# Kernel tuning notes

Hardware: AMD Instinct MI355X
Metric: run time of the kernel (lower is better)

Reference implementation:

```python
import jax, jax.numpy as jnp
import numpy as np

H, KVH, D, R = 32, 8, 128, 32
MASK_OUT = 0.5
NEG = -1e9  # stand-in for finfo.min to avoid -inf accumulation; preserves ordering/softmax
ROPE_THETA = 10000.0


def _rope_tables(S, D):
    inv = 1.0 / (ROPE_THETA ** (np.arange(0, D, 2, dtype=np.float32) / D))
    t = np.arange(S, dtype=np.float32)
    freqs = np.outer(t, inv)
    emb = np.concatenate([freqs, freqs], axis=-1)  # [S, D]
    return jnp.asarray(np.cos(emb)), jnp.asarray(np.sin(emb))


def _apply_rope(x, cos, sin):
    # x: [B,H,S,D]; cos/sin: [S,D]
    x1, x2 = jnp.split(x, 2, axis=-1)
    rot = jnp.concatenate([-x2, x1], axis=-1)
    return x * cos[None, None] + rot * sin[None, None]


def setup_inputs() -> dict:
    B, S, E = 1, 1024, 4096
    key = jax.random.key(0)
    ks = jax.random.split(key, 9)
    n = lambda k, shp, sc=0.02: jax.random.normal(k, shp, jnp.float32) * sc
    return {
        'hidden_states': n(ks[0], (B, S, E), 1.0),
        'wq': n(ks[1], (E, H * D)),
        'wk': n(ks[2], (E, KVH * D)),
        'wv': n(ks[3], (E, KVH * D)),
        'wo': n(ks[4], (H * D, E)),
        'mixq': n(ks[5], (E, R)),
        'mixk': n(ks[6], (E, R)),
        'q_pos': n(ks[7], (S, H, R, D)),
        'k_pos': n(ks[8], (S, H, R, D)),
    }


def reference(hidden_states, wq, wk, wv, wo, mixq, mixk, q_pos, k_pos):
    B, S, E = hidden_states.shape
    rep = H // KVH
    # QKV projections -> [B, heads, S, D]
    q = (hidden_states @ wq).reshape(B, S, H, D).transpose(0, 2, 1, 3)
    k = (hidden_states @ wk).reshape(B, S, KVH, D).transpose(0, 2, 1, 3)
    v = (hidden_states @ wv).reshape(B, S, KVH, D).transpose(0, 2, 1, 3)
    k = jnp.repeat(k, rep, axis=1)  # repeat_kv (GQA expand) -> [B,H,S,D]
    v = jnp.repeat(v, rep, axis=1)

    cos, sin = _rope_tables(S, D)
    qr = _apply_rope(q, cos, sin)
    kr = _apply_rope(k, cos, sin)
    scale = 1.0 / jnp.sqrt(jnp.float32(D))
    true_score = jnp.einsum('bhqd,bhkd->bhqk', qr, kr) * scale  # [B,H,S,S]

    # low-rank position-dependent draft score
    lrq = hidden_states @ mixq  # [B,S,R]
    lrk = hidden_states @ mixk
    pq = jnp.einsum('bmr,mhrd->bhmd', lrq, q_pos)  # [B,H,S,D]
    pk = jnp.einsum('bnr,nhrd->bhnd', lrk, k_pos)
    draft_score = jnp.einsum('bhqd,bhkd->bhqk', pq, pk)  # [B,H,S,S]

    causal = jnp.where(jnp.tril(jnp.ones((S, S), dtype=bool)), 0.0, NEG).astype(jnp.float32)[None, None]
    draft_score = draft_score + causal  # prefill: add causal mask to draft score

    num_remain = S - int(S * MASK_OUT)
    _, draft_idx = jax.lax.top_k(draft_score, num_remain)  # [B,H,S,K]

    # scatter 0 at kept kv positions, NEG elsewhere
    bi = jnp.arange(B)[:, None, None, None]
    hi = jnp.arange(H)[None, :, None, None]
    qi = jnp.arange(S)[None, None, :, None]
    topk_mask = jnp.full((B, H, S, S), NEG, jnp.float32).at[bi, hi, qi, draft_idx].set(0.0)

    probs = jax.nn.softmax(true_score + causal + topk_mask, axis=-1)
    out = jnp.einsum('bhqk,bhkd->bqhd', probs, v).reshape(B, S, H * D)
    return out @ wo
```

## Files before the change

### kernel.cpp

```cpp
#include <hip/hip_runtime.h>
#include <hip/hip_bf16.h>
#include <math.h>


typedef unsigned short u16;
typedef unsigned long long u64;
using bf16x8 = __attribute__((ext_vector_type(8))) short;
using f32x4  = __attribute__((ext_vector_type(4))) float;

#define NEGBIG -1e30f
#define QSCALE 0.08838834764831845f

__device__ __forceinline__ unsigned int fkey(float f) {
    unsigned int u = __float_as_uint(f);
    return (u & 0x80000000u) ? ~u : (u | 0x80000000u);
}

__device__ __forceinline__ u16 f2b(float f) {
    union { float f; unsigned u; } x; x.f = f;
    unsigned r = x.u + 0x7fffu + ((x.u >> 16) & 1u);
    return (u16)(r >> 16);
}

__device__ __forceinline__ void gl_lds16(const u16* g, u16* l) {
    __builtin_amdgcn_global_load_lds(
        (__attribute__((address_space(1))) void*)(g),
        (__attribute__((address_space(3))) void*)(l), 16, 0, 0);
}

__device__ __forceinline__ void rope_table_calc(int row, int i,
    float* __restrict__ cosb, float* __restrict__ sinb)
{
    double inv = pow(10000.0, -((double)(2 * i)) / 128.0);
    double ang = (double)row * inv;
    cosb[row * 64 + i] = (float)cos(ang);
    sinb[row * 64 + i] = (float)sin(ang);
}

__global__ __launch_bounds__(256) void init_kernel(
    const float* __restrict__ hs, u16* __restrict__ hs_bf,
    float* __restrict__ cosb, float* __restrict__ sinb)
{
    int bx = blockIdx.x, t = threadIdx.x;
    if (bx < 4096) {
        int i = bx * 256 + t;
        float4 v = ((const float4*)hs)[i];
        u16 o[4] = {f2b(v.x), f2b(v.y), f2b(v.z), f2b(v.w)};
        ((uint2*)hs_bf)[i] = *(const uint2*)o;
    } else {
        rope_table_calc((bx - 4096) * 4 + (t >> 6), t & 63, cosb, sinb);
    }
}

__device__ __forceinline__ void transpose_tile(
    const float* __restrict__ in, u16* __restrict__ out, int Kdim, int N,
    int bx, int by)
{
    __shared__ u16 tile[64][66];
    int n0 = bx * 64, k0 = by * 64;
    int t = threadIdx.x;
#pragma unroll
    for (int u = 0; u < 16; ++u) {
        int e = u * 256 + t; int r = e >> 6, c = e & 63;
        tile[r][c] = f2b(in[(size_t)(k0 + r) * N + n0 + c]);
    }
    __syncthreads();
#pragma unroll
    for (int u = 0; u < 16; ++u) {
        int e = u * 256 + t; int r = e >> 6, c = e & 63;
        out[(size_t)(n0 + r) * Kdim + k0 + c] = tile[c][r];
    }
}

__global__ __launch_bounds__(256) void transpose_bf16_kernel(
    const float* __restrict__ in, u16* __restrict__ out, int Kdim, int N)
{
    transpose_tile(in, out, Kdim, N, blockIdx.x, blockIdx.y);
}

__global__ __launch_bounds__(256) void transpose_qkvw_kernel(
    const float* __restrict__ wq, const float* __restrict__ wk, const float* __restrict__ wv,
    u16* __restrict__ wqT, u16* __restrict__ wkT, u16* __restrict__ wvT)
{
    int bx = blockIdx.x;
    const float* in; u16* outp; int N;
    if (bx < 64)      { in = wq; outp = wqT; N = 4096; }
    else if (bx < 80) { in = wk; outp = wkT; N = 1024; bx -= 64; }
    else              { in = wv; outp = wvT; N = 1024; bx -= 80; }
    transpose_tile(in, outp, 4096, N, bx, blockIdx.y);
}

__global__ __launch_bounds__(256) void init_fused_kernel(
    const float* __restrict__ hs, u16* __restrict__ hs_bf,
    float* __restrict__ cosb, float* __restrict__ sinb,
    const float* __restrict__ mixq, const float* __restrict__ mixk,
    float* __restrict__ lrq, float* __restrict__ lrk,
    const float* __restrict__ wq, const float* __restrict__ wk, const float* __restrict__ wv,
    u16* __restrict__ wqT, u16* __restrict__ wkT, u16* __restrict__ wvT)
{
    __shared__ float row[4096];
    __shared__ float part[2][32][4];
    int bx = blockIdx.x, t = threadIdx.x;
    if (bx < 4096) {
        int i = bx * 256 + t;
        float4 v = ((const float4*)hs)[i];
        u16 o[4] = {f2b(v.x), f2b(v.y), f2b(v.z), f2b(v.w)};
        ((uint2*)hs_bf)[i] = *(const uint2*)o;
    } else if (bx < 4352) {
        rope_table_calc((bx - 4096) * 4 + (t >> 6), t & 63, cosb, sinb);
    } else if (bx < 5376) {
        int m = bx - 4352;
#pragma unroll
        for (int u = 0; u < 4; ++u)
            ((float4*)row)[t + u * 256] = ((const float4*)(hs + (size_t)m * 4096))[t + u * 256];
        __syncthreads();
        int r = t & 31, which = (t >> 5) & 1, quarter = t >> 6;
        const float* mix = which ? mixk : mixq;
        float acc = 0.f;
        int kbase = quarter * 1024;
#pragma unroll 8
        for (int kk = 0; kk < 1024; ++kk)
            acc = fmaf(row[kbase + kk], mix[(size_t)(kbase + kk) * 32 + r], acc);
        part[which][r][quarter] = acc;
        __syncthreads();
        if (t < 64) {
            int r2 = t & 31, w2 = t >> 5;
            float s = part[w2][r2][0] + part[w2][r2][1] + part[w2][r2][2] + part[w2][r2][3];
            (w2 ? lrk : lrq)[(size_t)m * 32 + r2] = s;
        }
    } else {
        int idx = bx - 5376;
        int bxT = idx % 96, byT = idx / 96;
        const float* in; u16* outp; int N;
        if (bxT < 64)      { in = wq; outp = wqT; N = 4096; }
        else if (bxT < 80) { in = wk; outp = wkT; N = 1024; bxT -= 64; }
        else               { in = wv; outp = wvT; N = 1024; bxT -= 80; }
        transpose_tile(in, outp, 4096, N, bxT, byT);
    }
}

__global__ __launch_bounds__(128) void rope_pack2_kernel(
    const float* __restrict__ qb, const float* __restrict__ kb,
    const float* __restrict__ cosb, const float* __restrict__ sinb,
    u16* __restrict__ qr, u16* __restrict__ kr)
{
    int s = blockIdx.x, h = blockIdx.y, d = threadIdx.x;
    const float* src; u16* dst; int W; float scale;
    if (h < 32) { src = qb; dst = qr; W = 4096; scale = QSCALE; }
    else        { h -= 32; src = kb; dst = kr; W = 1024; scale = 1.0f; }
    float x  = src[(size_t)s * W + h * 128 + d];
    float x2 = src[(size_t)s * W + h * 128 + (d ^ 64)];
    float cs = cosb[s * 64 + (d & 63)];
    float sn = sinb[s * 64 + (d & 63)];
    float rot = (d < 64) ? -x2 : x2;
    dst[((size_t)h * 1024 + s) * 128 + d] = f2b((x * cs + rot * sn) * scale);
}

__global__ __launch_bounds__(256) void reduce_rope_v_kernel(
    const float* __restrict__ C0, const float* __restrict__ C1,
    const float* __restrict__ cosb, const float* __restrict__ sinb,
    u16* __restrict__ qr, u16* __restrict__ kr, u16* __restrict__ vT)
{
    __shared__ u16 tile[64][66];
    int bx = blockIdx.x, t = threadIdx.x;
    if (bx < 20480) {
        int sp = bx & 511, h40 = bx >> 9;
        int s = sp * 2 + (t >> 7), d = t & 127;
        int col; u16* dst; float scale;
        if (h40 < 32) { col = h40 * 128 + d; dst = qr + ((size_t)h40 * 1024 + s) * 128 + d; scale = QSCALE; }
        else { col = 4096 + (h40 - 32) * 128 + d; dst = kr + ((size_t)(h40 - 32) * 1024 + s) * 128 + d; scale = 1.0f; }
        int colp = col ^ 64;
        float x  = C0[(size_t)s * 6144 + col]  + C1[(size_t)s * 6144 + col];
        float x2 = C0[(size_t)s * 6144 + colp] + C1[(size_t)s * 6144 + colp];
        float cs = cosb[s * 64 + (d & 63)];
        float sn = sinb[s * 64 + (d & 63)];
        float rot = (d < 64) ? -x2 : x2;
        *dst = f2b((x * cs + rot * sn) * scale);
    } else {
        int idx = bx - 20480;
        int bxT = idx & 15, byT = idx >> 4;
        int n0 = bxT * 64, k0 = byT * 64;
#pragma unroll
        for (int u = 0; u < 16; ++u) {
            int e = u * 256 + t; int r = e >> 6, c = e & 63;
            size_t off = (size_t)(k0 + r) * 6144 + 5120 + n0 + c;
            tile[r][c] = f2b(C0[off] + C1[off]);
        }
        __syncthreads();
#pragma unroll
        for (int u = 0; u < 16; ++u) {
            int e = u * 256 + t; int r = e >> 6, c = e & 63;
            vT[(size_t)(n0 + r) * 1024 + k0 + c] = tile[c][r];
        }
    }
}

__global__ __launch_bounds__(256) void reduce_out_kernel(
    const float* __restrict__ D0, const float* __restrict__ D1, float* __restrict__ out)
{
    int i = blockIdx.x * 256 + threadIdx.x;
    float4 a = ((const float4*)D0)[i];
    float4 b = ((const float4*)D1)[i];
    ((float4*)out)[i] = make_float4(a.x + b.x, a.y + b.y, a.z + b.z, a.w + b.w);
}

__device__ __forceinline__ void gemm_bf16_panel(
    const u16* __restrict__ Ap,
    const u16* __restrict__ Bp,
    float* __restrict__ Cp,
    int Kdim, int kbase, int klen, int Cst)
{
    __shared__ u16 As[128 * 32];
    __shared__ u16 Bs[128 * 32];
    const int t = threadIdx.x;
    const int wave = t >> 6, lane = t & 63;
    const int wr = wave >> 1, wc = wave & 1;
    const int fr = lane & 15, fq = lane >> 4;

    f32x4 acc[4][4];
#pragma unroll
    for (int m = 0; m < 4; ++m)
#pragma unroll
        for (int n = 0; n < 4; ++n) acc[m][n] = 0.f;

    const int srow = 32 * wave + (lane >> 2);
    const int skc = (lane & 3) * 8;
    const u16* aS = Ap + (size_t)srow * Kdim + kbase + skc;
    const u16* bS = Bp + (size_t)srow * Kdim + kbase + skc;
    u16* aD0 = As + 1024 * wave;  u16* aD1 = aD0 + 512;
    u16* bD0 = Bs + 1024 * wave;  u16* bD1 = bD0 + 512;

    const int aoff = (wr * 64 + fr) * 32 + fq * 8;
    const int boff = (wc * 64 + fr) * 32 + fq * 8;

    for (int k0 = 0; k0 < klen; k0 += 32) {
        __syncthreads();
        gl_lds16(aS + k0, aD0);
        gl_lds16(aS + (size_t)16 * Kdim + k0, aD1);
        gl_lds16(bS + k0, bD0);
        gl_lds16(bS + (size_t)16 * Kdim + k0, bD1);
        __syncthreads();

        bf16x8 af[4], bfr[4];
#pragma unroll
        for (int m = 0; m < 4; ++m) af[m] = *(const bf16x8*)(As + aoff + m * 512);
#pragma unroll
        for (int n = 0; n < 4; ++n) bfr[n] = *(const bf16x8*)(Bs + boff + n * 512);
#pragma unroll
        for (int m = 0; m < 4; ++m)
#pragma unroll
            for (int n = 0; n < 4; ++n)
                acc[m][n] = __builtin_amdgcn_mfma_f32_16x16x32_bf16(af[m], bfr[n], acc[m][n], 0, 0, 0);
    }

    float* Cb = Cp + (size_t)(wr * 64 + fq * 4) * Cst + wc * 64 + fr;
#pragma unroll
    for (int m = 0; m < 4; ++m)
#pragma unroll
        for (int j = 0; j < 4; ++j)
#pragma unroll
            for (int n = 0; n < 4; ++n)
                Cb[(size_t)(m * 16 + j) * Cst + n * 16] = acc[m][n][j];
}

__global__ __launch_bounds__(256) void gemm_qkv_bf16_kernel(
    const u16* __restrict__ hs_bf, const u16* __restrict__ wqT,
    const u16* __restrict__ wkT, const u16* __restrict__ wvT,
    float* __restrict__ q, float* __restrict__ k, float* __restrict__ v)
{
    int bn = blockIdx.x, bm = blockIdx.y;
    const u16* Bsel; float* Csel; int Ncols;
    if (bn < 32)      { Bsel = wqT; Csel = q; Ncols = 4096; }
    else if (bn < 40) { Bsel = wkT; Csel = k; Ncols = 1024; bn -= 32; }
    else              { Bsel = wvT; Csel = v; Ncols = 1024; bn -= 40; }
    gemm_bf16_panel(hs_bf + (size_t)bm * 128 * 4096, Bsel + (size_t)bn * 128 * 4096,
                    Csel + (size_t)bm * 128 * Ncols + bn * 128, 4096, 0, 4096, Ncols);
}

__global__ __launch_bounds__(256) void gemm_wo_bf16_kernel(
    const u16* __restrict__ attn_bf, const u16* __restrict__ woT, float* __restrict__ out)
{
    int bn = blockIdx.x, bm = blockIdx.y;
    gemm_bf16_panel(attn_bf + (size_t)bm * 128 * 4096, woT + (size_t)bn * 128 * 4096,
                    out + (size_t)bm * 128 * 4096 + bn * 128, 4096, 0, 4096, 4096);
}

__global__ __launch_bounds__(256) void gemm_qkv_sk_kernel(
    const u16* __restrict__ hs_bf, const u16* __restrict__ wqT,
    const u16* __restrict__ wkT, const u16* __restrict__ wvT,
    float* __restrict__ C0, float* __restrict__ C1)
{
    int bn = blockIdx.x, bm = blockIdx.y, g = blockIdx.z;
    const u16* Bsel; int bnrow;
    if (bn < 32)      { Bsel = wqT; bnrow = bn; }
    else if (bn < 40) { Bsel = wkT; bnrow = bn - 32; }
    else              { Bsel = wvT; bnrow = bn - 40; }
    float* C = g ? C1 : C0;
    gemm_bf16_panel(hs_bf + (size_t)bm * 128 * 4096, Bsel + (size_t)bnrow * 128 * 4096,
                    C + (size_t)bm * 128 * 6144 + bn * 128, 4096, g * 2048, 2048, 6144);
}

__global__ __launch_bounds__(256) void gemm_wo_sk_kernel(
    const u16* __restrict__ attn_bf, const u16* __restrict__ woT,
    float* __restrict__ D0, float* __restrict__ D1)
{
    int bn = blockIdx.x, bm = blockIdx.y, g = blockIdx.z;
    float* C = g ? D1 : D0;
    gemm_bf16_panel(attn_bf + (size_t)bm * 128 * 4096, woT + (size_t)bn * 128 * 4096,
                    C + (size_t)bm * 128 * 4096 + bn * 128, 4096, g * 2048, 2048, 4096);
}

__global__ __launch_bounds__(256) void lr_kernel(
    const float* __restrict__ hs, const float* __restrict__ mixq, const float* __restrict__ mixk,
    float* __restrict__ lrq, float* __restrict__ lrk)
{
    __shared__ float row[4096];
    __shared__ float part[2][32][4];
    int m = blockIdx.x, t = threadIdx.x;
#pragma unroll
    for (int u = 0; u < 4; ++u)
        ((float4*)row)[t + u * 256] = ((const float4*)(hs + (size_t)m * 4096))[t + u * 256];
    __syncthreads();
    int r = t & 31, which = (t >> 5) & 1, quarter = t >> 6;
    const float* mix = which ? mixk : mixq;
    float acc = 0.f;
    int kbase = quarter * 1024;
#pragma unroll 8
    for (int kk = 0; kk < 1024; ++kk)
        acc = fmaf(row[kbase + kk], mix[(size_t)(kbase + kk) * 32 + r], acc);
    part[which][r][quarter] = acc;
    __syncthreads();
    if (t < 64) {
        int r2 = t & 31, w2 = t >> 5;
        float s = part[w2][r2][0] + part[w2][r2][1] + part[w2][r2][2] + part[w2][r2][3];
        (w2 ? lrk : lrq)[(size_t)m * 32 + r2] = s;
    }
}

__global__ __launch_bounds__(128) void ppos2_kernel(
    const float* __restrict__ lrq, const float* __restrict__ lrk,
    const float* __restrict__ qpos, const float* __restrict__ kpos,
    float* __restrict__ pq, float* __restrict__ pk)
{
    int h = blockIdx.x, by = blockIdx.y, d = threadIdx.x;
    const float* lr; const float* pos; float* outp; int m;
    if (by < 512) { m = 512 + by; lr = lrq; pos = qpos; outp = pq; }
    else          { m = by - 512; lr = lrk; pos = kpos; outp = pk; }
    __shared__ float lrs[32];
    if (d < 32) lrs[d] = lr[(size_t)m * 32 + d];
    __syncthreads();
    const float* base = pos + ((size_t)(m * 32 + h) * 32) * 128 + d;
    float acc = 0.f;
#pragma unroll
    for (int r = 0; r < 32; ++r)
        acc = fmaf(lrs[r], base[(size_t)r * 128], acc);
    outp[((size_t)h * 1024 + m) * 128 + d] = acc;
}

__global__ __launch_bounds__(256) void draft_gemm_kernel(
    const float* __restrict__ pq, const float* __restrict__ pk,
    float* __restrict__ scores, int h0)
{
    int idx = blockIdx.x;
    int bm, bc;
    if (idx < 10)      { bm = 4; bc = idx; }
    else if (idx < 22) { bm = 5; bc = idx - 10; }
    else if (idx < 36) { bm = 6; bc = idx - 22; }
    else               { bm = 7; bc = idx - 36; }
    int hh = blockIdx.y;

    const float* A  = pq + ((size_t)(h0 + hh) * 1024 + bm * 128) * 128;
    const float* BT = pk + ((size_t)(h0 + hh) * 1024 + bc * 64) * 128;
    float* C = scores + ((size_t)hh * 512 + (bm - 4) * 128) * 1024 + bc * 64;

    __shared__ float As[8][128];
    __shared__ float Bs[8][64];
    const int t = threadIdx.x;
    const int tx = t & 15, ty = (t >> 4) & 15;

    float acc[8][4];
#pragma unroll
    for (int u = 0; u < 8; ++u)
#pragma unroll
        for (int w = 0; w < 4; ++w) acc[u][w] = 0.f;

    const int ai = t >> 1, ah = (t & 1) * 4;
    const int bi = t >> 2, bh = (t & 3) * 2;
    const float* Ap = A + (size_t)ai * 128 + ah;
    const float* Bp = BT + (size_t)bi * 128 + bh;

    for (int k0 = 0; k0 < 128; k0 += 8) {
        float4 av = *(const float4*)(Ap + k0);
        float2 bv = *(const float2*)(Bp + k0);
        __syncthreads();
        As[ah + 0][ai] = av.x; As[ah + 1][ai] = av.y;
        As[ah + 2][ai] = av.z; As[ah + 3][ai] = av.w;
        Bs[bh][bi] = bv.x; Bs[bh + 1][bi] = bv.y;
        __syncthreads();
#pragma unroll
        for (int kk = 0; kk < 8; ++kk) {
            float4 a0 = *(const float4*)(&As[kk][ty * 4]);
            float4 a1 = *(const float4*)(&As[kk][64 + ty * 4]);
            float4 b0 = *(const float4*)(&Bs[kk][tx * 4]);
            float aa[8] = {a0.x, a0.y, a0.z, a0.w, a1.x, a1.y, a1.z, a1.w};
#pragma unroll
            for (int u = 0; u < 8; ++u) {
                acc[u][0] = fmaf(aa[u], b0.x, acc[u][0]);
                acc[u][1] = fmaf(aa[u], b0.y, acc[u][1]);
                acc[u][2] = fmaf(aa[u], b0.z, acc[u][2]);
                acc[u][3] = fmaf(aa[u], b0.w, acc[u][3]);
            }
        }
    }
#pragma unroll
    for (int u = 0; u < 8; ++u) {
        int row = (u < 4) ? (ty * 4 + u) : (64 + ty * 4 + (u - 4));
        *(float4*)(C + (size_t)row * 1024 + tx * 4)
            = make_float4(acc[u][0], acc[u][1], acc[u][2], acc[u][3]);
    }
}

__global__ __launch_bounds__(256) void topk_select_kernel(
    const float* __restrict__ scores, int h0,
    unsigned long long* __restrict__ mask)
{
    int qt = blockIdx.x, hh = blockIdx.y;
    int h = h0 + hh;
    int t = threadIdx.x;
    const int i = t >> 4, jj = t & 15;
    const int lrow = qt * 16 + i;
    const int qrow = 512 + lrow;

    const float* src = scores + ((size_t)hh * 512 + lrow) * 1024;

    unsigned int vals[64];
#pragma unroll
    for (int g = 0; g < 16; ++g) {
        float4 v = *(const float4*)(src + g * 64 + jj * 4);
        int col = g * 64 + jj * 4;
        vals[g * 4 + 0] = fkey((col + 0) <= qrow ? v.x : NEGBIG);
        vals[g * 4 + 1] = fkey((col + 1) <= qrow ? v.y : NEGBIG);
        vals[g * 4 + 2] = fkey((col + 2) <= qrow ? v.z : NEGBIG);
        vals[g * 4 + 3] = fkey((col + 3) <= qrow ? v.w : NEGBIG);
    }

    unsigned int p = 0u;
    int kth = 512;
    for (int b = 31; b >= 0; --b) {
        unsigned int bit = 1u << b;
        unsigned int himask = (b == 31) ? 0u : (0xFFFFFFFFu << (b + 1));
        int cnt = 0;
#pragma unroll
        for (int n = 0; n < 64; ++n)
            cnt += (int)((((vals[n] ^ p) & himask) == 0u) && ((vals[n] & bit) != 0u));
        cnt += __shfl_xor(cnt, 1);
        cnt += __shfl_xor(cnt, 2);
        cnt += __shfl_xor(cnt, 4);
        cnt += __shfl_xor(cnt, 8);
        if (cnt >= kth) p |= bit; else kth -= cnt;
    }

    unsigned long long wpart[16];
#pragma unroll
    for (int w = 0; w < 16; ++w) wpart[w] = 0ull;
#pragma unroll
    for (int g = 0; g < 16; ++g)
#pragma unroll
        for (int e = 0; e < 4; ++e)
            wpart[g] |= ((unsigned long long)(vals[g * 4 + e] >= p)) << (4 * jj + e);
#pragma unroll
    for (int s = 1; s < 16; s <<= 1) {
#pragma unroll
        for (int w = 0; w < 16; ++w)
            wpart[w] |= __shfl_xor(wpart[w], s);
    }
    mask[((size_t)h * 1024 + qrow) * 16 + jj] = wpart[jj];
}

#define ATTN_KP 136
#define ATTN_VP 72

__global__ __launch_bounds__(256) void attn_mfma_kernel(
    const u16* __restrict__ qr, const u16* __restrict__ kr,
    const u16* __restrict__ vT,
    const unsigned long long* __restrict__ mask,
    u16* __restrict__ attn)
{
    int bx = blockIdx.x;
    int qt = (bx & 1) ? (bx >> 1) : (15 - (bx >> 1));
    int h = blockIdx.y;
    int kvh = h >> 2;
    int q0 = qt * 64;
    int t = threadIdx.x;
    int wave = t >> 6, lane = t & 63;
    int fr = lane & 15, fq = lane >> 4;
    int qrow = q0 + wave * 16 + fr;

    __shared__ u16 Ks[64 * ATTN_KP];
    __shared__ u16 Vs[128 * ATTN_VP];

    bf16x8 qf[4];
    const u16* qbase = qr + ((size_t)h * 1024 + qrow) * 128 + fq * 8;
#pragma unroll
    for (int kc = 0; kc < 4; ++kc)
        qf[kc] = *(const bf16x8*)(qbase + kc * 32);

    float m_run = -3.0e38f, l_run = 0.f;
    f32x4 accO[8];
#pragma unroll
    for (int m2 = 0; m2 < 8; ++m2) accO[m2] = 0.f;

    const unsigned long long* mrow = mask + ((size_t)h * 1024 + qrow) * 16;
    const bool use_mask = (qrow >= 512);
    const u16* kgh = kr + (size_t)kvh * 1024 * 128;
    const u16* vgh = vT + (size_t)kvh * 128 * 1024;

    int ntiles = qt + 1;
    for (int c = 0; c < ntiles; ++c) {
        int kv0 = c * 64;
        __syncthreads();
#pragma unroll
        for (int u = 0; u < 4; ++u) {
            int e = t + u * 256;
            int row = e >> 4, bc2 = (e & 15) * 8;
            uint4 d4 = *(const uint4*)(kgh + ((size_t)(kv0 + row)) * 128 + bc2);
            *(uint4*)(&Ks[row * ATTN_KP + bc2]) = d4;
        }
#pragma unroll
        for (int u = 0; u < 4; ++u) {
            int e = t + u * 256;
            int row = e >> 3, bc2 = (e & 7) * 8;
            uint4 d4 = *(const uint4*)(vgh + (size_t)row * 1024 + kv0 + bc2);
            *(uint4*)(&Vs[row * ATTN_VP + bc2]) = d4;
        }
        __syncthreads();

        f32x4 accS[4];
        accS[0] = 0.f; accS[1] = 0.f; accS[2] = 0.f; accS[3] = 0.f;
#pragma unroll
        for (int t2 = 0; t2 < 4; ++t2)
#pragma unroll
            for (int kc = 0; kc < 4; ++kc) {
                bf16x8 kf = *(const bf16x8*)(&Ks[(t2 * 16 + fr) * ATTN_KP + kc * 32 + fq * 8]);
                accS[t2] = __builtin_amdgcn_mfma_f32_16x16x32_bf16(kf, qf[kc], accS[t2], 0, 0, 0);
            }

        unsigned long long mw = use_mask ? mrow[c] : ~0ull;
        float p[4][4];
        float tmax = -3.0e38f;
#pragma unroll
        for (int t2 = 0; t2 < 4; ++t2)
#pragma unroll
            for (int j = 0; j < 4; ++j) {
                int kvi = (t2 << 4) + (fq << 2) + j;
                bool ok = ((mw >> kvi) & 1ull) && (kv0 + kvi <= qrow);
                float s = ok ? accS[t2][j] : -3.0e38f;
                p[t2][j] = s;
                tmax = fmaxf(tmax, s);
            }
// ... 5 lines not shown
#pragma unroll
        for (int t2 = 0; t2 < 4; ++t2)
#pragma unroll
            for (int j = 0; j < 4; ++j) {
                float e = (p[t2][j] > -1.0e38f) ? __expf(p[t2][j] - m_new) : 0.f;
                p[t2][j] = e;
                psum += e;
            }
        psum += __shfl_xor(psum, 16);
        psum += __shfl_xor(psum, 32);
        l_run = l_run * sf + psum;
        m_run = m_new;

#pragma unroll
        for (int m2 = 0; m2 < 8; ++m2) accO[m2] *= sf;

        union { uint4 u; bf16x8 b; } pc[2];
        int srcA = fr + ((fq & 1) << 5);
        int srcB = srcA + 16;
        bool hi = (fq & 2) != 0;
#pragma unroll
        for (int half = 0; half < 2; ++half) {
            unsigned W0, W1, W2, W3;
            asm("v_cvt_pk_bf16_f32 %0, %1, %2" : "=v"(W0) : "v"(p[2 * half][0]),     "v"(p[2 * half][1]));
            asm("v_cvt_pk_bf16_f32 %0, %1, %2" : "=v"(W1) : "v"(p[2 * half][2]),     "v"(p[2 * half][3]));
            asm("v_cvt_pk_bf16_f32 %0, %1, %2" : "=v"(W2) : "v"(p[2 * half + 1][0]), "v"(p[2 * half + 1][1]));
            asm("v_cvt_pk_bf16_f32 %0, %1, %2" : "=v"(W3) : "v"(p[2 * half + 1][2]), "v"(p[2 * half + 1][3]));
            unsigned a0 = __shfl(W0, srcA), a1 = __shfl(W1, srcA);
            unsigned a2 = __shfl(W2, srcA), a3 = __shfl(W3, srcA);
            unsigned b0 = __shfl(W0, srcB), b1 = __shfl(W1, srcB);
            unsigned b2 = __shfl(W2, srcB), b3 = __shfl(W3, srcB);
            pc[half].u.x = hi ? a2 : a0;
            pc[half].u.y = hi ? a3 : a1;
            pc[half].u.z = hi ? b2 : b0;
            pc[half].u.w = hi ? b3 : b1;
        }

#pragma unroll
        for (int m2 = 0; m2 < 8; ++m2) {
            bf16x8 vf0 = *(const bf16x8*)(&Vs[(m2 * 16 + fr) * ATTN_VP + fq * 8]);
            accO[m2] = __builtin_amdgcn_mfma_f32_16x16x32_bf16(vf0, pc[0].b, accO[m2], 0, 0, 0);
            bf16x8 vf1 = *(const bf16x8*)(&Vs[(m2 * 16 + fr) * ATTN_VP + 32 + fq * 8]);
            accO[m2] = __builtin_amdgcn_mfma_f32_16x16x32_bf16(vf1, pc[1].b, accO[m2], 0, 0, 0);
        }
    }

    float il = 1.0f / l_run;
    u16* obase = attn + (size_t)qrow * 4096 + h * 128 + fq * 4;
#pragma unroll
    for (int m2 = 0; m2 < 8; ++m2) {
        uint2 st;
        st.x = (unsigned)f2b(accO[m2][0] * il) | ((unsigned)f2b(accO[m2][1] * il) << 16);
        st.y = (unsigned)f2b(accO[m2][2] * il) | ((unsigned)f2b(accO[m2][3] * il) << 16);
        *(uint2*)(obase + m2 * 16) = st;
    }
}

extern "C" void kernel_launch(void* const* d_in, const int* in_sizes, int n_in,
                              void* d_out, int out_size, void* d_ws, size_t ws_size,
                              hipStream_t stream)
{
    (void)in_sizes; (void)n_in; (void)out_size;
    const float* hs   = (const float*)d_in[0];
    const float* wq   = (const float*)d_in[1];
    const float* wk   = (const float*)d_in[2];
    const float* wv   = (const float*)d_in[3];
    const float* wo   = (const float*)d_in[4];
    const float* mixq = (const float*)d_in[5];
    const float* mixk = (const float*)d_in[6];
    const float* qpos = (const float*)d_in[7];
    const float* kpos = (const float*)d_in[8];
    float* out = (float*)d_out;
    char* B = (char*)d_ws;
    const size_t MB = 1ull << 20;

    if (ws_size >= 123 * MB) {
        u16* hs_bf = (u16*)(B);
        u16* wkT   = (u16*)(B + 8 * MB);
        u16* wvT   = (u16*)(B + 16 * MB);
        u16* wqT   = (u16*)(B + 24 * MB);
        u16* qr    = (u16*)(B + 24 * MB);
        u16* kr    = (u16*)(B + 32 * MB);
        u16* vT    = (u16*)(B + 34 * MB);
        u16* woT   = (u16*)(B + 24 * MB);
        float* C0  = (float*)(B + 56 * MB);
        float* C1  = (float*)(B + 80 * MB);
        float* pq  = (float*)(B + 56 * MB);
        float* pk  = (float*)(B + 72 * MB);
        float* scores = (float*)(B + 88 * MB);
        float* D0  = (float*)(B + 56 * MB);
        float* D1  = (float*)(B + 72 * MB);
        u64* mask  = (u64*)(B + 120 * MB);
        float* lrq = (float*)(B + 122 * MB);
        float* lrk = lrq + 32768;
        float* cosb = lrk + 32768;
        float* sinb = cosb + 65536;
        u16* attn_bf = hs_bf;

        hipLaunchKernelGGL(init_fused_kernel, dim3(11520), dim3(256), 0, stream,
                           hs, hs_bf, cosb, sinb, mixq, mixk, lrq, lrk,
                           wq, wk, wv, wqT, wkT, wvT);
        hipLaunchKernelGGL(gemm_qkv_sk_kernel, dim3(48, 8, 2), dim3(256), 0, stream,
                           hs_bf, wqT, wkT, wvT, C0, C1);
        hipLaunchKernelGGL(reduce_rope_v_kernel, dim3(20736), dim3(256), 0, stream,
                           C0, C1, cosb, sinb, qr, kr, vT);
        hipLaunchKernelGGL(ppos2_kernel, dim3(32, 1536), dim3(128), 0, stream,
                           lrq, lrk, qpos, kpos, pq, pk);
        for (int h0 = 0; h0 < 32; h0 += 16) {
            hipLaunchKernelGGL(draft_gemm_kernel, dim3(52, 16), dim3(256), 0, stream,
                               pq, pk, scores, h0);
            hipLaunchKernelGGL(topk_select_kernel, dim3(32, 16), dim3(256), 0, stream,
                               scores, h0, mask);
        }
        hipLaunchKernelGGL(attn_mfma_kernel, dim3(16, 32), dim3(256), 0, stream,
                           qr, kr, vT, mask, attn_bf);
        hipLaunchKernelGGL(transpose_bf16_kernel, dim3(64, 64), dim3(256), 0, stream,
                           wo, woT, 4096, 4096);
        hipLaunchKernelGGL(gemm_wo_sk_kernel, dim3(32, 8, 2), dim3(256), 0, stream,
                           attn_bf, woT, D0, D1);
        hipLaunchKernelGGL(reduce_out_kernel, dim3(4096), dim3(256), 0, stream,
                           D0, D1, out);
    } else {
        float* ws   = (float*)d_ws;
        float* qb   = ws;
        float* kb   = qb + 4194304;
        float* vb   = kb + 1048576;
        float* pq   = vb + 1048576;
        float* pk   = pq + 4194304;
        float* lrq  = pk + 4194304;
        float* lrk  = lrq + 32768;
        float* cosb = lrk + 32768;
        float* sinb = cosb + 65536;
        u64* mask = (u64*)(sinb + 65536);
        u16* hs_bf = (u16*)(ws + 14876672 + 1048576);
        u16* wkT   = hs_bf + 4194304;
        u16* wvT   = wkT + 4194304;
        u16* wqT   = (u16*)pq;
        u16* woT   = (u16*)pq;
        u16* qr_bf = (u16*)pq;
        u16* kr_bf = (u16*)pk;
        u16* vT_bf = (u16*)(pk + 1048576);
        u16* attn_bf = hs_bf;
        float* scores = (float*)hs_bf;

        hipLaunchKernelGGL(init_kernel, dim3(4352), dim3(256), 0, stream, hs, hs_bf, cosb, sinb);
        hipLaunchKernelGGL(transpose_qkvw_kernel, dim3(96, 64), dim3(256), 0, stream,
                           wq, wk, wv, wqT, wkT, wvT);
        hipLaunchKernelGGL(gemm_qkv_bf16_kernel, dim3(48, 8), dim3(256), 0, stream,
                           hs_bf, wqT, wkT, wvT, qb, kb, vb);
        hipLaunchKernelGGL(lr_kernel, dim3(1024), dim3(256), 0, stream, hs, mixq, mixk, lrq, lrk);
        hipLaunchKernelGGL(ppos2_kernel, dim3(32, 1536), dim3(128), 0, stream,
                           lrq, lrk, qpos, kpos, pq, pk);
        for (int h0 = 0; h0 < 32; h0 += 8) {
            hipLaunchKernelGGL(draft_gemm_kernel, dim3(52, 8), dim3(256), 0, stream,
                               pq, pk, scores, h0);
            hipLaunchKernelGGL(topk_select_kernel, dim3(32, 8), dim3(256), 0, stream,
                               scores, h0, mask);
        }
        hipLaunchKernelGGL(rope_pack2_kernel, dim3(1024, 40), dim3(128), 0, stream,
                           qb, kb, cosb, sinb, qr_bf, kr_bf);
        hipLaunchKernelGGL(transpose_bf16_kernel, dim3(16, 16), dim3(256), 0, stream,
                           vb, vT_bf, 1024, 1024);
        hipLaunchKernelGGL(attn_mfma_kernel, dim3(16, 32), dim3(256), 0, stream,
                           qr_bf, kr_bf, vT_bf, mask, attn_bf);
        hipLaunchKernelGGL(transpose_bf16_kernel, dim3(64, 64), dim3(256), 0, stream,
                           wo, woT, 4096, 4096);
        hipLaunchKernelGGL(gemm_wo_bf16_kernel, dim3(32, 8), dim3(256), 0, stream,
                           attn_bf, woT, out);
    }
}
```

Baseline: 692.7 us.

## Fuse QKV GEMM with position projection and overlap draft scoring with rope/transposes

Replaces the split-K QKV GEMM plus separate ppos kernel with one heterogeneous launch that runs the unsplit QKV GEMM alongside the pq/pk position projections. The rope/V-transpose work and the wo transpose are folded into launches that also compute draft-score tiles. Draft scoring and top-k now run in four 8-head chunks with a smaller scores buffer, and the workspace layout is reshuffled to match. The goal is fewer launches and better occupancy by overlapping independent work. The cost is heterogeneous blocks sharing one LDS and register budget, and 384 full-K GEMM blocks that may form a long tail.

```diff
diff --git a/kernel.cpp b/kernel.cpp
--- a/kernel.cpp
+++ b/kernel.cpp
@@ -35,6 +35,32 @@
     double ang = (double)row * inv;
     cosb[row * 64 + i] = (float)cos(ang);
     sinb[row * 64 + i] = (float)sin(ang);
+}
+
+__device__ __forceinline__ void transpose_tile(
+    const float* __restrict__ in, u16* __restrict__ out, int Kdim, int N,
+    int bx, int by)
+{
+    __shared__ u16 tile[64][66];
+    int n0 = bx * 64, k0 = by * 64;
+    int t = threadIdx.x;
+#pragma unroll
+    for (int u = 0; u < 16; ++u) {
+        int e = u * 256 + t; int r = e >> 6, c = e & 63;
+        tile[r][c] = f2b(in[(size_t)(k0 + r) * N + n0 + c]);
+    }
+    __syncthreads();
+#pragma unroll
+    for (int u = 0; u < 16; ++u) {
+        int e = u * 256 + t; int r = e >> 6, c = e & 63;
+        out[(size_t)(n0 + r) * Kdim + k0 + c] = tile[c][r];
+    }
+}
+
+__global__ __launch_bounds__(256) void transpose_bf16_kernel(
+    const float* __restrict__ in, u16* __restrict__ out, int Kdim, int N)
+{
+    transpose_tile(in, out, Kdim, N, blockIdx.x, blockIdx.y);
 }
 
 __global__ __launch_bounds__(256) void init_kernel(
@@ -52,32 +78,6 @@
     }
 }
 
-__device__ __forceinline__ void transpose_tile(
-    const float* __restrict__ in, u16* __restrict__ out, int Kdim, int N,
-    int bx, int by)
-{
-    __shared__ u16 tile[64][66];
-    int n0 = bx * 64, k0 = by * 64;
-    int t = threadIdx.x;
-#pragma unroll
-    for (int u = 0; u < 16; ++u) {
-        int e = u * 256 + t; int r = e >> 6, c = e & 63;
-        tile[r][c] = f2b(in[(size_t)(k0 + r) * N + n0 + c]);
-    }
-    __syncthreads();
-#pragma unroll
-    for (int u = 0; u < 16; ++u) {
-        int e = u * 256 + t; int r = e >> 6, c = e & 63;
-        out[(size_t)(n0 + r) * Kdim + k0 + c] = tile[c][r];
-    }
-}
-
-__global__ __launch_bounds__(256) void transpose_bf16_kernel(
-    const float* __restrict__ in, u16* __restrict__ out, int Kdim, int N)
-{
-    transpose_tile(in, out, Kdim, N, blockIdx.x, blockIdx.y);
-}
-
 __global__ __launch_bounds__(256) void transpose_qkvw_kernel(
     const float* __restrict__ wq, const float* __restrict__ wk, const float* __restrict__ wv,
     u16* __restrict__ wqT, u16* __restrict__ wkT, u16* __restrict__ wvT)
@@ -88,55 +88,6 @@
     else if (bx < 80) { in = wk; outp = wkT; N = 1024; bx -= 64; }
     else              { in = wv; outp = wvT; N = 1024; bx -= 80; }
     transpose_tile(in, outp, 4096, N, bx, blockIdx.y);
-}
-
-__global__ __launch_bounds__(256) void init_fused_kernel(
-    const float* __restrict__ hs, u16* __restrict__ hs_bf,
-    float* __restrict__ cosb, float* __restrict__ sinb,
-    const float* __restrict__ mixq, const float* __restrict__ mixk,
-    float* __restrict__ lrq, float* __restrict__ lrk,
-    const float* __restrict__ wq, const float* __restrict__ wk, const float* __restrict__ wv,
-    u16* __restrict__ wqT, u16* __restrict__ wkT, u16* __restrict__ wvT)
-{
-    __shared__ float row[4096];
-    __shared__ float part[2][32][4];
-    int bx = blockIdx.x, t = threadIdx.x;
-    if (bx < 4096) {
-        int i = bx * 256 + t;
-        float4 v = ((const float4*)hs)[i];
-        u16 o[4] = {f2b(v.x), f2b(v.y), f2b(v.z), f2b(v.w)};
-        ((uint2*)hs_bf)[i] = *(const uint2*)o;
-    } else if (bx < 4352) {
-        rope_table_calc((bx - 4096) * 4 + (t >> 6), t & 63, cosb, sinb);
-    } else if (bx < 5376) {
-        int m = bx - 4352;
-#pragma unroll
-        for (int u = 0; u < 4; ++u)
-            ((float4*)row)[t + u * 256] = ((const float4*)(hs + (size_t)m * 4096))[t + u * 256];
-        __syncthreads();
-        int r = t & 31, which = (t >> 5) & 1, quarter = t >> 6;
-        const float* mix = which ? mixk : mixq;
-        float acc = 0.f;
-        int kbase = quarter * 1024;
-#pragma unroll 8
-        for (int kk = 0; kk < 1024; ++kk)
-            acc = fmaf(row[kbase + kk], mix[(size_t)(kbase + kk) * 32 + r], acc);
-        part[which][r][quarter] = acc;
-        __syncthreads();
-        if (t < 64) {
-            int r2 = t & 31, w2 = t >> 5;
-            float s = part[w2][r2][0] + part[w2][r2][1] + part[w2][r2][2] + part[w2][r2][3];
-            (w2 ? lrk : lrq)[(size_t)m * 32 + r2] = s;
-        }
-    } else {
-        int idx = bx - 5376;
-        int bxT = idx % 96, byT = idx / 96;
-        const float* in; u16* outp; int N;
-        if (bxT < 64)      { in = wq; outp = wqT; N = 4096; }
-        else if (bxT < 80) { in = wk; outp = wkT; N = 1024; bxT -= 64; }
-        else               { in = wv; outp = wvT; N = 1024; bxT -= 80; }
-        transpose_tile(in, outp, 4096, N, bxT, byT);
-    }
 }
 
 __global__ __launch_bounds__(128) void rope_pack2_kernel(
@@ -154,160 +105,6 @@
     float sn = sinb[s * 64 + (d & 63)];
     float rot = (d < 64) ? -x2 : x2;
     dst[((size_t)h * 1024 + s) * 128 + d] = f2b((x * cs + rot * sn) * scale);
-}
-
-__global__ __launch_bounds__(256) void reduce_rope_v_kernel(
-    const float* __restrict__ C0, const float* __restrict__ C1,
-    const float* __restrict__ cosb, const float* __restrict__ sinb,
-    u16* __restrict__ qr, u16* __restrict__ kr, u16* __restrict__ vT)
-{
-    __shared__ u16 tile[64][66];
-    int bx = blockIdx.x, t = threadIdx.x;
-    if (bx < 20480) {
-        int sp = bx & 511, h40 = bx >> 9;
-        int s = sp * 2 + (t >> 7), d = t & 127;
-        int col; u16* dst; float scale;
-        if (h40 < 32) { col = h40 * 128 + d; dst = qr + ((size_t)h40 * 1024 + s) * 128 + d; scale = QSCALE; }
-        else { col = 4096 + (h40 - 32) * 128 + d; dst = kr + ((size_t)(h40 - 32) * 1024 + s) * 128 + d; scale = 1.0f; }
-        int colp = col ^ 64;
-        float x  = C0[(size_t)s * 6144 + col]  + C1[(size_t)s * 6144 + col];
-        float x2 = C0[(size_t)s * 6144 + colp] + C1[(size_t)s * 6144 + colp];
-        float cs = cosb[s * 64 + (d & 63)];
-        float sn = sinb[s * 64 + (d & 63)];
-        float rot = (d < 64) ? -x2 : x2;
-        *dst = f2b((x * cs + rot * sn) * scale);
-    } else {
-        int idx = bx - 20480;
-        int bxT = idx & 15, byT = idx >> 4;
-        int n0 = bxT * 64, k0 = byT * 64;
-#pragma unroll
-        for (int u = 0; u < 16; ++u) {
-            int e = u * 256 + t; int r = e >> 6, c = e & 63;
-            size_t off = (size_t)(k0 + r) * 6144 + 5120 + n0 + c;
-            tile[r][c] = f2b(C0[off] + C1[off]);
-        }
-        __syncthreads();
-#pragma unroll
-        for (int u = 0; u < 16; ++u) {
-            int e = u * 256 + t; int r = e >> 6, c = e & 63;
-            vT[(size_t)(n0 + r) * 1024 + k0 + c] = tile[c][r];
-        }
-    }
-}
-
-__global__ __launch_bounds__(256) void reduce_out_kernel(
-    const float* __restrict__ D0, const float* __restrict__ D1, float* __restrict__ out)
-{
-    int i = blockIdx.x * 256 + threadIdx.x;
-    float4 a = ((const float4*)D0)[i];
-    float4 b = ((const float4*)D1)[i];
-    ((float4*)out)[i] = make_float4(a.x + b.x, a.y + b.y, a.z + b.z, a.w + b.w);
-}
-
-__device__ __forceinline__ void gemm_bf16_panel(
-    const u16* __restrict__ Ap,
-    const u16* __restrict__ Bp,
-    float* __restrict__ Cp,
-    int Kdim, int kbase, int klen, int Cst)
-{
-    __shared__ u16 As[128 * 32];
-    __shared__ u16 Bs[128 * 32];
-    const int t = threadIdx.x;
-    const int wave = t >> 6, lane = t & 63;
-    const int wr = wave >> 1, wc = wave & 1;
-    const int fr = lane & 15, fq = lane >> 4;
-
-    f32x4 acc[4][4];
-#pragma unroll
-    for (int m = 0; m < 4; ++m)
-#pragma unroll
-        for (int n = 0; n < 4; ++n) acc[m][n] = 0.f;
-
-    const int srow = 32 * wave + (lane >> 2);
-    const int skc = (lane & 3) * 8;
-    const u16* aS = Ap + (size_t)srow * Kdim + kbase + skc;
-    const u16* bS = Bp + (size_t)srow * Kdim + kbase + skc;
-    u16* aD0 = As + 1024 * wave;  u16* aD1 = aD0 + 512;
-    u16* bD0 = Bs + 1024 * wave;  u16* bD1 = bD0 + 512;
-
-    const int aoff = (wr * 64 + fr) * 32 + fq * 8;
-    const int boff = (wc * 64 + fr) * 32 + fq * 8;
-
-    for (int k0 = 0; k0 < klen; k0 += 32) {
-        __syncthreads();
-        gl_lds16(aS + k0, aD0);
-        gl_lds16(aS + (size_t)16 * Kdim + k0, aD1);
-        gl_lds16(bS + k0, bD0);
-        gl_lds16(bS + (size_t)16 * Kdim + k0, bD1);
-        __syncthreads();
-
-        bf16x8 af[4], bfr[4];
-#pragma unroll
-        for (int m = 0; m < 4; ++m) af[m] = *(const bf16x8*)(As + aoff + m * 512);
-#pragma unroll
-        for (int n = 0; n < 4; ++n) bfr[n] = *(const bf16x8*)(Bs + boff + n * 512);
-#pragma unroll
-        for (int m = 0; m < 4; ++m)
-#pragma unroll
-            for (int n = 0; n < 4; ++n)
-                acc[m][n] = __builtin_amdgcn_mfma_f32_16x16x32_bf16(af[m], bfr[n], acc[m][n], 0, 0, 0);
-    }
-
-    float* Cb = Cp + (size_t)(wr * 64 + fq * 4) * Cst + wc * 64 + fr;
-#pragma unroll
-    for (int m = 0; m < 4; ++m)
-#pragma unroll
-        for (int j = 0; j < 4; ++j)
-#pragma unroll
-            for (int n = 0; n < 4; ++n)
-                Cb[(size_t)(m * 16 + j) * Cst + n * 16] = acc[m][n][j];
-}
-
-__global__ __launch_bounds__(256) void gemm_qkv_bf16_kernel(
-    const u16* __restrict__ hs_bf, const u16* __restrict__ wqT,
-    const u16* __restrict__ wkT, const u16* __restrict__ wvT,
-    float* __restrict__ q, float* __restrict__ k, float* __restrict__ v)
-{
-    int bn = blockIdx.x, bm = blockIdx.y;
-    const u16* Bsel; float* Csel; int Ncols;
-    if (bn < 32)      { Bsel = wqT; Csel = q; Ncols = 4096; }
-    else if (bn < 40) { Bsel = wkT; Csel = k; Ncols = 1024; bn -= 32; }
-    else              { Bsel = wvT; Csel = v; Ncols = 1024; bn -= 40; }
-    gemm_bf16_panel(hs_bf + (size_t)bm * 128 * 4096, Bsel + (size_t)bn * 128 * 4096,
-                    Csel + (size_t)bm * 128 * Ncols + bn * 128, 4096, 0, 4096, Ncols);
-}
-
-__global__ __launch_bounds__(256) void gemm_wo_bf16_kernel(
-    const u16* __restrict__ attn_bf, const u16* __restrict__ woT, float* __restrict__ out)
-{
-    int bn = blockIdx.x, bm = blockIdx.y;
-    gemm_bf16_panel(attn_bf + (size_t)bm * 128 * 4096, woT + (size_t)bn * 128 * 4096,
-                    out + (size_t)bm * 128 * 4096 + bn * 128, 4096, 0, 4096, 4096);
-}
-
-__global__ __launch_bounds__(256) void gemm_qkv_sk_kernel(
-    const u16* __restrict__ hs_bf, const u16* __restrict__ wqT,
-    const u16* __restrict__ wkT, const u16* __restrict__ wvT,
-    float* __restrict__ C0, float* __restrict__ C1)
-{
-    int bn = blockIdx.x, bm = blockIdx.y, g = blockIdx.z;
-    const u16* Bsel; int bnrow;
-    if (bn < 32)      { Bsel = wqT; bnrow = bn; }
-    else if (bn < 40) { Bsel = wkT; bnrow = bn - 32; }
-    else              { Bsel = wvT; bnrow = bn - 40; }
-    float* C = g ? C1 : C0;
-    gemm_bf16_panel(hs_bf + (size_t)bm * 128 * 4096, Bsel + (size_t)bnrow * 128 * 4096,
-                    C + (size_t)bm * 128 * 6144 + bn * 128, 4096, g * 2048, 2048, 6144);
-}
-
-__global__ __launch_bounds__(256) void gemm_wo_sk_kernel(
-    const u16* __restrict__ attn_bf, const u16* __restrict__ woT,
-    float* __restrict__ D0, float* __restrict__ D1)
-{
-    int bn = blockIdx.x, bm = blockIdx.y, g = blockIdx.z;
-    float* C = g ? D1 : D0;
-    gemm_bf16_panel(attn_bf + (size_t)bm * 128 * 4096, woT + (size_t)bn * 128 * 4096,
-                    C + (size_t)bm * 128 * 4096 + bn * 128, 4096, g * 2048, 2048, 4096);
 }
 
 __global__ __launch_bounds__(256) void lr_kernel(
@@ -357,21 +154,224 @@
     outp[((size_t)h * 1024 + m) * 128 + d] = acc;
 }
 
-__global__ __launch_bounds__(256) void draft_gemm_kernel(
+__global__ __launch_bounds__(256) void init_fused_kernel(
+    const float* __restrict__ hs, u16* __restrict__ hs_bf,
+    float* __restrict__ cosb, float* __restrict__ sinb,
+    const float* __restrict__ mixq, const float* __restrict__ mixk,
+    float* __restrict__ lrq, float* __restrict__ lrk,
+    const float* __restrict__ wq, const float* __restrict__ wk, const float* __restrict__ wv,
+    u16* __restrict__ wqT, u16* __restrict__ wkT, u16* __restrict__ wvT)
+{
+    __shared__ float row[4096];
+    __shared__ float part[2][32][4];
+    int bx = blockIdx.x, t = threadIdx.x;
+    if (bx < 4096) {
+        int i = bx * 256 + t;
+        float4 v = ((const float4*)hs)[i];
+        u16 o[4] = {f2b(v.x), f2b(v.y), f2b(v.z), f2b(v.w)};
+        ((uint2*)hs_bf)[i] = *(const uint2*)o;
+    } else if (bx < 4352) {
+        rope_table_calc((bx - 4096) * 4 + (t >> 6), t & 63, cosb, sinb);
+    } else if (bx < 5376) {
+        int m = bx - 4352;
+#pragma unroll
+        for (int u = 0; u < 4; ++u)
+            ((float4*)row)[t + u * 256] = ((const float4*)(hs + (size_t)m * 4096))[t + u * 256];
+        __syncthreads();
+        int r = t & 31, which = (t >> 5) & 1, quarter = t >> 6;
+        const float* mix = which ? mixk : mixq;
+        float acc = 0.f;
+        int kbase = quarter * 1024;
+#pragma unroll 8
+        for (int kk = 0; kk < 1024; ++kk)
+            acc = fmaf(row[kbase + kk], mix[(size_t)(kbase + kk) * 32 + r], acc);
+        part[which][r][quarter] = acc;
+        __syncthreads();
+        if (t < 64) {
+            int r2 = t & 31, w2 = t >> 5;
+            float s = part[w2][r2][0] + part[w2][r2][1] + part[w2][r2][2] + part[w2][r2][3];
+            (w2 ? lrk : lrq)[(size_t)m * 32 + r2] = s;
+        }
+    } else {
+        int idx = bx - 5376;
+        int bxT = idx % 96, byT = idx / 96;
+        const float* in; u16* outp; int N;
+        if (bxT < 64)      { in = wq; outp = wqT; N = 4096; }
+        else if (bxT < 80) { in = wk; outp = wkT; N = 1024; bxT -= 64; }
+        else               { in = wv; outp = wvT; N = 1024; bxT -= 80; }
+        transpose_tile(in, outp, 4096, N, bxT, byT);
+    }
+}
+
+__device__ __forceinline__ void gemm_bf16_panel(
+    const u16* __restrict__ Ap, const u16* __restrict__ Bp,
+    float* __restrict__ Cp, int Kdim, int kbase, int klen, int Cst)
+{
+    __shared__ u16 As[128 * 32];
+    __shared__ u16 Bs[128 * 32];
+    const int t = threadIdx.x;
+    const int wave = t >> 6, lane = t & 63;
+    const int wr = wave >> 1, wc = wave & 1;
+    const int fr = lane & 15, fq = lane >> 4;
+
+    f32x4 acc[4][4];
+#pragma unroll
+    for (int m = 0; m < 4; ++m)
+#pragma unroll
+        for (int n = 0; n < 4; ++n) acc[m][n] = 0.f;
+
+    const int srow = 32 * wave + (lane >> 2);
+    const int skc = (lane & 3) * 8;
+    const u16* aS = Ap + (size_t)srow * Kdim + kbase + skc;
+    const u16* bS = Bp + (size_t)srow * Kdim + kbase + skc;
+    u16* aD0 = As + 1024 * wave;  u16* aD1 = aD0 + 512;
+    u16* bD0 = Bs + 1024 * wave;  u16* bD1 = bD0 + 512;
+
+    const int aoff = (wr * 64 + fr) * 32 + fq * 8;
+    const int boff = (wc * 64 + fr) * 32 + fq * 8;
+
+    for (int k0 = 0; k0 < klen; k0 += 32) {
+        __syncthreads();
+        gl_lds16(aS + k0, aD0);
+        gl_lds16(aS + (size_t)16 * Kdim + k0, aD1);
+        gl_lds16(bS + k0, bD0);
+        gl_lds16(bS + (size_t)16 * Kdim + k0, bD1);
+        __syncthreads();
+
+        bf16x8 af[4], bfr[4];
+#pragma unroll
+        for (int m = 0; m < 4; ++m) af[m] = *(const bf16x8*)(As + aoff + m * 512);
+#pragma unroll
+        for (int n = 0; n < 4; ++n) bfr[n] = *(const bf16x8*)(Bs + boff + n * 512);
+#pragma unroll
+        for (int m = 0; m < 4; ++m)
+#pragma unroll
+            for (int n = 0; n < 4; ++n)
+                acc[m][n] = __builtin_amdgcn_mfma_f32_16x16x32_bf16(af[m], bfr[n], acc[m][n], 0, 0, 0);
+    }
+
+    float* Cb = Cp + (size_t)(wr * 64 + fq * 4) * Cst + wc * 64 + fr;
+#pragma unroll
+    for (int m = 0; m < 4; ++m)
+#pragma unroll
+        for (int j = 0; j < 4; ++j)
+#pragma unroll
+            for (int n = 0; n < 4; ++n)
+                Cb[(size_t)(m * 16 + j) * Cst + n * 16] = acc[m][n][j];
+}
+
+__global__ __launch_bounds__(256) void gemm_qkv_bf16_kernel(
+    const u16* __restrict__ hs_bf, const u16* __restrict__ wqT,
+    const u16* __restrict__ wkT, const u16* __restrict__ wvT,
+    float* __restrict__ q, float* __restrict__ k, float* __restrict__ v)
+{
+    int bn = blockIdx.x, bm = blockIdx.y;
+    const u16* Bsel; float* Csel; int Ncols;
+    if (bn < 32)      { Bsel = wqT; Csel = q; Ncols = 4096; }
+    else if (bn < 40) { Bsel = wkT; Csel = k; Ncols = 1024; bn -= 32; }
+    else              { Bsel = wvT; Csel = v; Ncols = 1024; bn -= 40; }
+    gemm_bf16_panel(hs_bf + (size_t)bm * 128 * 4096, Bsel + (size_t)bn * 128 * 4096,
+                    Csel + (size_t)bm * 128 * Ncols + bn * 128, 4096, 0, 4096, Ncols);
+}
+
+__global__ __launch_bounds__(256) void gemm_wo_bf16_kernel(
+    const u16* __restrict__ attn_bf, const u16* __restrict__ woT, float* __restrict__ out)
+{
+    int bn = blockIdx.x, bm = blockIdx.y;
+    gemm_bf16_panel(attn_bf + (size_t)bm * 128 * 4096, woT + (size_t)bn * 128 * 4096,
+                    out + (size_t)bm * 128 * 4096 + bn * 128, 4096, 0, 4096, 4096);
+}
+
+__global__ __launch_bounds__(256) void qkv_ppos_kernel(
+    const u16* __restrict__ hs_bf, const u16* __restrict__ wqT,
+    const u16* __restrict__ wkT, const u16* __restrict__ wvT,
+    float* __restrict__ C,
+    const float* __restrict__ lrq, const float* __restrict__ lrk,
+    const float* __restrict__ qpos, const float* __restrict__ kpos,
+    float* __restrict__ pq, float* __restrict__ pk)
+{
+    int bx = blockIdx.x, t = threadIdx.x;
+    if (bx < 384) {
+        int bn = bx % 48, bm = bx / 48;
+        const u16* Bsel; int bnrow;
+        if (bn < 32)      { Bsel = wqT; bnrow = bn; }
+        else if (bn < 40) { Bsel = wkT; bnrow = bn - 32; }
+        else              { Bsel = wvT; bnrow = bn - 40; }
+        gemm_bf16_panel(hs_bf + (size_t)bm * 128 * 4096, Bsel + (size_t)bnrow * 128 * 4096,
+                        C + (size_t)bm * 128 * 6144 + bn * 128, 4096, 0, 4096, 6144);
+    } else {
+        int idx = bx - 384;
+        int bp = idx >> 5, h = idx & 31;
+        int sub = t >> 7, d = t & 127;
+        int by = bp * 2 + sub;
+        const float* lr; const float* pos; float* outp; int m;
+        if (by < 512) { m = 512 + by; lr = lrq; pos = qpos; outp = pq; }
+        else          { m = by - 512; lr = lrk; pos = kpos; outp = pk; }
+        __shared__ float lrs[2][32];
+        if (d < 32) lrs[sub][d] = lr[(size_t)m * 32 + d];
+        __syncthreads();
+        const float* base = pos + ((size_t)(m * 32 + h) * 32) * 128 + d;
+        float acc = 0.f;
+#pragma unroll
+        for (int r = 0; r < 32; ++r)
+            acc = fmaf(lrs[sub][r], base[(size_t)r * 128], acc);
+        outp[((size_t)h * 1024 + m) * 128 + d] = acc;
+    }
+}
+
+__device__ __forceinline__ void reduce_rope_item(
+    const float* __restrict__ C,
+    const float* __restrict__ cosb, const float* __restrict__ sinb,
+    u16* __restrict__ qr, u16* __restrict__ kr, int bx)
+{
+    int t = threadIdx.x;
+    int sp = bx & 511, h40 = bx >> 9;
+    int s = sp * 2 + (t >> 7), d = t & 127;
+    int col; u16* dst; float scale;
+    if (h40 < 32) { col = h40 * 128 + d; dst = qr + ((size_t)h40 * 1024 + s) * 128 + d; scale = QSCALE; }
+    else { col = 4096 + (h40 - 32) * 128 + d; dst = kr + ((size_t)(h40 - 32) * 1024 + s) * 128 + d; scale = 1.0f; }
+    int colp = col ^ 64;
+    float x  = C[(size_t)s * 6144 + col];
+    float x2 = C[(size_t)s * 6144 + colp];
+    float cs = cosb[s * 64 + (d & 63)];
+    float sn = sinb[s * 64 + (d & 63)];
+    float rot = (d < 64) ? -x2 : x2;
+    *dst = f2b((x * cs + rot * sn) * scale);
+}
+
+__device__ __forceinline__ void v_transpose_dev(
+    const float* __restrict__ C, u16* __restrict__ vT, int idx)
+{
+    __shared__ u16 vtile[64][66];
+    int bxT = idx & 15, byT = idx >> 4;
+    int n0 = bxT * 64, k0 = byT * 64;
+    int t = threadIdx.x;
+#pragma unroll
+    for (int u = 0; u < 16; ++u) {
+        int e = u * 256 + t; int r = e >> 6, c = e & 63;
+        vtile[r][c] = f2b(C[(size_t)(k0 + r) * 6144 + 5120 + n0 + c]);
+    }
+    __syncthreads();
+#pragma unroll
+    for (int u = 0; u < 16; ++u) {
+        int e = u * 256 + t; int r = e >> 6, c = e & 63;
+        vT[(size_t)(n0 + r) * 1024 + k0 + c] = vtile[c][r];
+    }
+}
+
+__device__ __forceinline__ void draft_tile_compute(
     const float* __restrict__ pq, const float* __restrict__ pk,
-    float* __restrict__ scores, int h0)
-{
-    int idx = blockIdx.x;
+    float* __restrict__ scores, int h0, int idx, int hh)
+{
     int bm, bc;
     if (idx < 10)      { bm = 4; bc = idx; }
     else if (idx < 22) { bm = 5; bc = idx - 10; }
     else if (idx < 36) { bm = 6; bc = idx - 22; }
     else               { bm = 7; bc = idx - 36; }
-    int hh = blockIdx.y;
 
     const float* A  = pq + ((size_t)(h0 + hh) * 1024 + bm * 128) * 128;
     const float* BT = pk + ((size_t)(h0 + hh) * 1024 + bc * 64) * 128;
-    float* C = scores + ((size_t)hh * 512 + (bm - 4) * 128) * 1024 + bc * 64;
+    float* Cs = scores + ((size_t)hh * 512 + (bm - 4) * 128) * 1024 + bc * 64;
 
     __shared__ float As[8][128];
     __shared__ float Bs[8][64];
@@ -415,9 +415,37 @@
 #pragma unroll
     for (int u = 0; u < 8; ++u) {
         int row = (u < 4) ? (ty * 4 + u) : (64 + ty * 4 + (u - 4));
-        *(float4*)(C + (size_t)row * 1024 + tx * 4)
+        *(float4*)(Cs + (size_t)row * 1024 + tx * 4)
             = make_float4(acc[u][0], acc[u][1], acc[u][2], acc[u][3]);
     }
+}
+
+__global__ __launch_bounds__(256) void draft_gemm_kernel(
+    const float* __restrict__ pq, const float* __restrict__ pk,
+    float* __restrict__ scores, int h0)
+{
+    draft_tile_compute(pq, pk, scores, h0, blockIdx.x, blockIdx.y);
+}
+
+__global__ __launch_bounds__(256) void draft0_fused_kernel(
+    const float* __restrict__ pq, const float* __restrict__ pk,
+    float* __restrict__ scores, const float* __restrict__ C,
+    const float* __restrict__ cosb, const float* __restrict__ sinb,
+    u16* __restrict__ qr, u16* __restrict__ kr, u16* __restrict__ vT)
+{
+    int bx = blockIdx.x;
+    if (bx < 416) draft_tile_compute(pq, pk, scores, 0, bx % 52, bx / 52);
+    else if (bx < 416 + 20480) reduce_rope_item(C, cosb, sinb, qr, kr, bx - 416);
+    else v_transpose_dev(C, vT, bx - 416 - 20480);
+}
+
+__global__ __launch_bounds__(256) void draft1_fused_kernel(
+    const float* __restrict__ pq, const float* __restrict__ pk,
+    float* __restrict__ scores, const float* __restrict__ wo, u16* __restrict__ woT)
+{
+    int bx = blockIdx.x;
+    if (bx < 416) draft_tile_compute(pq, pk, scores, 8, bx % 52, bx / 52);
+    else { int i = bx - 416; transpose_tile(wo, woT, 4096, 4096, i & 63, i >> 6); }
 }
 
 __global__ __launch_bounds__(256) void topk_select_kernel(
@@ -475,6 +503,25 @@
             wpart[w] |= __shfl_xor(wpart[w], s);
     }
     mask[((size_t)h * 1024 + qrow) * 16 + jj] = wpart[jj];
+}
+
+__global__ __launch_bounds__(256) void gemm_wo_sk_kernel(
+    const u16* __restrict__ attn_bf, const u16* __restrict__ woT,
+    float* __restrict__ D0, float* __restrict__ D1)
+{
+    int bn = blockIdx.x, bm = blockIdx.y, g = blockIdx.z;
+    float* C = g ? D1 : D0;
+    gemm_bf16_panel(attn_bf + (size_t)bm * 128 * 4096, woT + (size_t)bn * 128 * 4096,
+                    C + (size_t)bm * 128 * 4096 + bn * 128, 4096, g * 2048, 2048, 4096);
+}
+
+__global__ __launch_bounds__(256) void reduce_out_kernel(
+    const float* __restrict__ D0, const float* __restrict__ D1, float* __restrict__ out)
+{
+    int i = blockIdx.x * 256 + threadIdx.x;
+    float4 a = ((const float4*)D0)[i];
+    float4 b = ((const float4*)D1)[i];
+    ((float4*)out)[i] = make_float4(a.x + b.x, a.y + b.y, a.z + b.z, a.w + b.w);
 }
 
 #define ATTN_KP 136
@@ -646,16 +693,15 @@
         u16* qr    = (u16*)(B + 24 * MB);
         u16* kr    = (u16*)(B + 32 * MB);
         u16* vT    = (u16*)(B + 34 * MB);
-        u16* woT   = (u16*)(B + 24 * MB);
-        float* C0  = (float*)(B + 56 * MB);
-        float* C1  = (float*)(B + 80 * MB);
-        float* pq  = (float*)(B + 56 * MB);
-        float* pk  = (float*)(B + 72 * MB);
-        float* scores = (float*)(B + 88 * MB);
-        float* D0  = (float*)(B + 56 * MB);
-        float* D1  = (float*)(B + 72 * MB);
-        u64* mask  = (u64*)(B + 120 * MB);
-        float* lrq = (float*)(B + 122 * MB);
+        float* scores = (float*)(B + 36 * MB);
+        u64* mask  = (u64*)(B + 52 * MB);
+        float* C   = (float*)(B + 56 * MB);
+        u16* woT   = (u16*)(B + 56 * MB);
+        float* pq  = (float*)(B + 88 * MB);
+        float* pk  = (float*)(B + 104 * MB);
+        float* D0  = (float*)(B + 88 * MB);
+        float* D1  = (float*)(B + 104 * MB);
+        float* lrq = (float*)(B + 120 * MB);
         float* lrk = lrq + 32768;
         float* cosb = lrk + 32768;
         float* sinb = cosb + 65536;
@@ -664,22 +710,26 @@
         hipLaunchKernelGGL(init_fused_kernel, dim3(11520), dim3(256), 0, stream,
                            hs, hs_bf, cosb, sinb, mixq, mixk, lrq, lrk,
                            wq, wk, wv, wqT, wkT, wvT);
-        hipLaunchKernelGGL(gemm_qkv_sk_kernel, dim3(48, 8, 2), dim3(256), 0, stream,
-                           hs_bf, wqT, wkT, wvT, C0, C1);
-        hipLaunchKernelGGL(reduce_rope_v_kernel, dim3(20736), dim3(256), 0, stream,
-                           C0, C1, cosb, sinb, qr, kr, vT);
-        hipLaunchKernelGGL(ppos2_kernel, dim3(32, 1536), dim3(128), 0, stream,
-                           lrq, lrk, qpos, kpos, pq, pk);
-        for (int h0 = 0; h0 < 32; h0 += 16) {
-            hipLaunchKernelGGL(draft_gemm_kernel, dim3(52, 16), dim3(256), 0, stream,
-                               pq, pk, scores, h0);
-            hipLaunchKernelGGL(topk_select_kernel, dim3(32, 16), dim3(256), 0, stream,
-                               scores, h0, mask);
-        }
+        hipLaunchKernelGGL(qkv_ppos_kernel, dim3(24960), dim3(256), 0, stream,
+                           hs_bf, wqT, wkT, wvT, C, lrq, lrk, qpos, kpos, pq, pk);
+        hipLaunchKernelGGL(draft0_fused_kernel, dim3(21152), dim3(256), 0, stream,
+                           pq, pk, scores, C, cosb, sinb, qr, kr, vT);
+        hipLaunchKernelGGL(topk_select_kernel, dim3(32, 8), dim3(256), 0, stream,
+                           scores, 0, mask);
+        hipLaunchKernelGGL(draft1_fused_kernel, dim3(4512), dim3(256), 0, stream,
+                           pq, pk, scores, wo, woT);
+        hipLaunchKernelGGL(topk_select_kernel, dim3(32, 8), dim3(256), 0, stream,
+                           scores, 8, mask);
+        hipLaunchKernelGGL(draft_gemm_kernel, dim3(52, 8), dim3(256), 0, stream,
+                           pq, pk, scores, 16);
+        hipLaunchKernelGGL(topk_select_kernel, dim3(32, 8), dim3(256), 0, stream,
+                           scores, 16, mask);
+        hipLaunchKernelGGL(draft_gemm_kernel, dim3(52, 8), dim3(256), 0, stream,
+                           pq, pk, scores, 24);
+        hipLaunchKernelGGL(topk_select_kernel, dim3(32, 8), dim3(256), 0, stream,
+                           scores, 24, mask);
         hipLaunchKernelGGL(attn_mfma_kernel, dim3(16, 32), dim3(256), 0, stream,
                            qr, kr, vT, mask, attn_bf);
-        hipLaunchKernelGGL(transpose_bf16_kernel, dim3(64, 64), dim3(256), 0, stream,
-                           wo, woT, 4096, 4096);
         hipLaunchKernelGGL(gemm_wo_sk_kernel, dim3(32, 8, 2), dim3(256), 0, stream,
                            attn_bf, woT, D0, D1);
         hipLaunchKernelGGL(reduce_out_kernel, dim3(4096), dim3(256), 0, stream,
```

Result: faster. 673.1 us (median of 2 runs) (-2.8%).
